# Optimization experiments

Measured on AMD Instinct MI355X. Metric: run time of the kernel, lower is better.

The kernel has to match this reference:

```python
import jax, jax.numpy as jnp
import numpy as np

B, L, NUM_AA, E, H = 128, 2048, 20, 16, 128

def _mlp(x, W1, b1, W2, b2, W3, b3):
    h = jax.nn.relu(x @ W1 + b1)
    h = jax.nn.relu(h @ W2 + b2)
    return h @ W3 + b3

def _mlp_params(key, in_dim):
    k1, k2, k3 = jax.random.split(key, 3)
    W1 = jax.random.normal(k1, (in_dim, H), jnp.float32) / np.sqrt(in_dim)
    W2 = jax.random.normal(k2, (H, H), jnp.float32) / np.sqrt(H)
    W3 = jax.random.normal(k3, (H, 1), jnp.float32) / np.sqrt(H)
    return W1, jnp.zeros((H,), jnp.float32), W2, jnp.zeros((H,), jnp.float32), W3, jnp.zeros((1,), jnp.float32)

def setup_inputs() -> dict:
    key = jax.random.key(0)
    kR, ks, ke, kl, kt, kp = jax.random.split(key, 6)
    inp = {
        'R': jax.random.normal(kR, (B, L, 3), jnp.float32) * 3.8,  # ~CA-CA scale
        'seq': jax.random.randint(ks, (B, L), 0, NUM_AA),
        'emb': jax.random.normal(ke, (NUM_AA, E), jnp.float32),
    }
    for pref, k, d in (('fl', kl, 1 + 2 * E), ('ft', kt, 1 + 3 * E), ('fp', kp, 2 + 4 * E)):
        W1, b1, W2, b2, W3, b3 = _mlp_params(k, d)
        inp.update({f'{pref}_W1': W1, f'{pref}_b1': b1, f'{pref}_W2': W2, f'{pref}_b2': b2, f'{pref}_W3': W3, f'{pref}_b3': b3})
    return inp

def _energy(R, e, fl, ft, fp):
    d = R[:, 1:, :] - R[:, :-1, :]                      # [B,L-1,3] bond vectors
    lengths = jnp.linalg.norm(d, axis=-1)               # [B,L-1]
    x_l = jnp.concatenate([lengths[..., None], e[:, :-1, :], e[:, 1:, :]], axis=-1)
    E_l = _mlp(x_l, *fl)[..., 0].sum(axis=1)
    # bond angles at atom i+1 between (R[i]-R[i+1]) and (R[i+2]-R[i+1])
    u, v = -d[:, :-1, :], d[:, 1:, :]                   # [B,L-2,3]
    cos_t = jnp.sum(u * v, axis=-1) / (jnp.linalg.norm(u, axis=-1) * jnp.linalg.norm(v, axis=-1))
    theta_in = jnp.clip(cos_t, -1.0, 1.0)               # use_cos_theta=True -> cos(arccos(clip))
    x_t = jnp.concatenate([theta_in[..., None], e[:, :-2, :], e[:, 1:-1, :], e[:, 2:, :]], axis=-1)
    E_t = _mlp(x_t, *ft)[..., 0].sum(axis=1)
    # torsions over quadruples
    b1, b2, b3 = d[:, :-2, :], d[:, 1:-1, :], d[:, 2:, :]
    n1 = jnp.cross(b1, b2)
    n2 = jnp.cross(b2, b3)
    b2u = b2 / jnp.linalg.norm(b2, axis=-1, keepdims=True)
    m1 = jnp.cross(n1, b2u)
    phi = jnp.arctan2(jnp.sum(m1 * n2, axis=-1), jnp.sum(n1 * n2, axis=-1))  # [B,L-3]
    sc = jnp.stack([jnp.sin(phi), jnp.cos(phi)], axis=-1)                    # [B,L-3,2]
    x_p = jnp.concatenate([sc, e[:, :-3, :], e[:, 1:-2, :], e[:, 2:-1, :], e[:, 3:, :]], axis=-1)
    E_p = _mlp(x_p, *fp)[..., 0].sum(axis=1)
    return E_l + E_t + E_p

def reference(R, seq, emb,
              fl_W1, fl_b1, fl_W2, fl_b2, fl_W3, fl_b3,
              ft_W1, ft_b1, ft_W2, ft_b2, ft_W3, ft_b3,
              fp_W1, fp_b1, fp_W2, fp_b2, fp_W3, fp_b3):
    e = emb[seq]                                        # [B,L,E]
    return _energy(R, e,
                   (fl_W1, fl_b1, fl_W2, fl_b2, fl_W3, fl_b3),
                   (ft_W1, ft_b1, ft_W2, ft_b2, ft_W3, ft_b3),
                   (fp_W1, fp_b1, fp_W2, fp_b2, fp_W3, fp_b3))
```

## Files before the change

kernel.cpp:

```cpp
#include <hip/hip_runtime.h>


typedef short bf16x8  __attribute__((ext_vector_type(8)));
typedef float f32x4   __attribute__((ext_vector_type(4)));
typedef float f32x16  __attribute__((ext_vector_type(16)));

constexpr int Lc = 2048;

union FragU { uint4 u; bf16x8 v; };

__device__ __forceinline__ unsigned short f2bf(float f) {
    union { float f; unsigned u; } v; v.f = f;
    unsigned u = v.u;
    u = u + 0x7FFFu + ((u >> 16) & 1u);
    return (unsigned short)(u >> 16);
}

__device__ __forceinline__ unsigned pkbf(float a, float b) {
    unsigned ua = __float_as_uint(a) + 0x8000u;
    unsigned ub = __float_as_uint(b) + 0x8000u;
    return __builtin_amdgcn_perm(ub, ua, 0x07060302u);
}

__device__ __forceinline__ void pl32swap(unsigned &a, unsigned &b) {
#if __has_builtin(__builtin_amdgcn_permlane32_swap)
    auto r = __builtin_amdgcn_permlane32_swap(a, b, false, false);
    a = r[0]; b = r[1];
#else
    asm("v_permlane32_swap_b32 %0, %1" : "+v"(a), "+v"(b));
#endif
}

__global__ __launch_bounds__(256)
void prep_kernel(const float* __restrict__ W1_0, const float* __restrict__ b1_0,
                 const float* __restrict__ W1_1, const float* __restrict__ b1_1,
                 const float* __restrict__ W1_2, const float* __restrict__ b1_2,
                 const float* __restrict__ W2_0, const float* __restrict__ W2_1,
                 const float* __restrict__ W2_2,
                 const float* __restrict__ emb, char* __restrict__ ws,
                 float* __restrict__ out)
{
    const int tid = blockIdx.x * 256 + threadIdx.x;
    const int np  = gridDim.x * 256;
    if (blockIdx.x == 0 && threadIdx.x < 128) out[threadIdx.x] = 0.0f;

    unsigned short* d2 = (unsigned short*)ws;
    for (int o = tid; o < 3 * 16384; o += np) {
        int t = o >> 14, r = o & 16383;
        int col = (r >> 3) & 127;
        int k   = ((r >> 10) << 3) | (r & 7);
        const float* W2 = (t == 0) ? W2_0 : (t == 1) ? W2_1 : W2_2;
        d2[o] = f2bf(W2[k * 128 + col]);
    }
    unsigned short* d1 = (unsigned short*)(ws + 98304);
    for (int o = tid; o < 3 * 12288; o += np) {
        int t = o / 12288, r = o - t * 12288;
        int hid = (r >> 3) & 127;
        int k   = ((r >> 10) << 3) | (r & 7);
        const int NE16 = (t == 0) ? 32 : (t == 1) ? 48 : 64;
        const int NG   = (t == 2) ? 2 : 1;
        const float* W1 = (t == 0) ? W1_0 : (t == 1) ? W1_1 : W1_2;
        const float* b1 = (t == 0) ? b1_0 : (t == 1) ? b1_1 : b1_2;
        float v = 0.0f;
        if (k >= 16) {
            int j = k - 16;
            if (j < NE16) v = W1[(NG + j) * 128 + hid];
        } else if (k == 4) v = b1[hid];
        else if (t == 0 && k == 0) v = W1_0[hid];
        else if (t == 1 && k == 1) v = W1_1[hid];
        else if (t == 2 && k == 2) v = W1_2[hid];
        else if (t == 2 && k == 3) v = W1_2[128 + hid];
        d1[o] = f2bf(v);
    }
    unsigned short* eb = (unsigned short*)(ws + 172032);
    for (int i = tid; i < 320; i += np) eb[i] = f2bf(emb[i]);
}

struct SMem {
    float  Rbuf[393];
    uint2  geomh[128];
    int    seqb[132];
    alignas(16) unsigned short ebuf[320];
    float  part[4];
};

template<int TYPE>
__device__ __forceinline__ void type_pass(
    const SMem& sm, const char* __restrict__ ws,
    const float* __restrict__ b2, const float* __restrict__ w3,
    int i0, int wv, int ln31, int hi, f32x4& p4)
{
    constexpr int NEMB  = (TYPE == 0) ? 2 : (TYPE == 1) ? 3 : 4;
    constexpr int STEPS = 1 + NEMB;
    constexpr int ROWSB = Lc - 1 - TYPE;

    const unsigned short* w1t = (const unsigned short*)(ws + 98304 + TYPE * 24576);
    const unsigned short* w2t = (const unsigned short*)(ws + TYPE * 32768);
    const int rloc = wv * 32 + ln31;

    f32x16 acc1[4];
    acc1[0] = (f32x16)(0.f); acc1[1] = (f32x16)(0.f);
    acc1[2] = (f32x16)(0.f); acc1[3] = (f32x16)(0.f);

#pragma unroll
    for (int s = 0; s < STEPS; ++s) {
        FragU bb;
        if (s == 0) {
            if (hi == 0) {
                uint2 g = sm.geomh[rloc];
                bb.u = make_uint4(g.x, g.y, 0x00003F80u, 0u);
            } else {
                bb.u = make_uint4(0u, 0u, 0u, 0u);
            }
        } else {
            bb.u = *(const uint4*)&sm.ebuf[sm.seqb[rloc + (s - 1)] * 16 + hi * 8];
        }
#pragma unroll
        for (int mt = 0; mt < 4; ++mt) {
            FragU A1;
            A1.u = *(const uint4*)&w1t[(((s * 2 + hi) * 128) + mt * 32 + ln31) * 8];
            acc1[mt] = __builtin_amdgcn_mfma_f32_32x32x16_bf16(A1.v, bb.v, acc1[mt], 0, 0, 0);
        }
    }

    FragU a2[8];
#pragma unroll
    for (int mt = 0; mt < 4; ++mt) {
        unsigned P0[4], P1[4];
#pragma unroll
        for (int g = 0; g < 4; ++g) {
            float v0 = fmaxf(acc1[mt][4 * g + 0], 0.f);
            float v1 = fmaxf(acc1[mt][4 * g + 1], 0.f);
            float v2 = fmaxf(acc1[mt][4 * g + 2], 0.f);
            float v3 = fmaxf(acc1[mt][4 * g + 3], 0.f);
            P0[g] = pkbf(v0, v1);
            P1[g] = pkbf(v2, v3);
        }
        unsigned a0 = P0[0], b0 = P0[1]; pl32swap(a0, b0);
        unsigned a1 = P1[0], b1 = P1[1]; pl32swap(a1, b1);
        a2[2 * mt].u     = make_uint4(a0, a1, b0, b1);
        unsigned c0 = P0[2], d0 = P0[3]; pl32swap(c0, d0);
        unsigned c1 = P1[2], d1 = P1[3]; pl32swap(c1, d1);
        a2[2 * mt + 1].u = make_uint4(c0, c1, d0, d1);
    }

    float b2v[4], w3v[4];
#pragma unroll
    for (int nt = 0; nt < 4; ++nt) {
        b2v[nt] = b2[nt * 32 + ln31];
        w3v[nt] = w3[nt * 32 + ln31];
    }

    f32x16 acc2[4];
    acc2[0] = (f32x16)(0.f); acc2[1] = (f32x16)(0.f);
    acc2[2] = (f32x16)(0.f); acc2[3] = (f32x16)(0.f);
#pragma unroll
    for (int s2 = 0; s2 < 8; ++s2) {
#pragma unroll
        for (int nt = 0; nt < 4; ++nt) {
            FragU B2;
            B2.u = *(const uint4*)&w2t[(((s2 * 2 + hi) * 128) + nt * 32 + ln31) * 8];
            acc2[nt] = __builtin_amdgcn_mfma_f32_32x32x16_bf16(a2[s2].v, B2.v, acc2[nt], 0, 0, 0);
        }
    }

    const f32x4 z4 = (f32x4){0.f, 0.f, 0.f, 0.f};
#pragma unroll
    for (int g = 0; g < 4; ++g) {
        const int rbase = i0 + wv * 32 + 8 * g + 4 * hi;
#pragma unroll
        for (int nt = 0; nt < 4; ++nt) {
            f32x4 v;
            v[0] = acc2[nt][4 * g + 0]; v[1] = acc2[nt][4 * g + 1];
            v[2] = acc2[nt][4 * g + 2]; v[3] = acc2[nt][4 * g + 3];
            v = __builtin_elementwise_max(v + b2v[nt], z4);
            if (rbase + 3 < ROWSB) {
                p4 += v * w3v[nt];
            } else {
#pragma unroll
                for (int j = 0; j < 4; ++j)
                    if (rbase + j < ROWSB) p4[j] += v[j] * w3v[nt];
            }
        }
    }
}

__global__ __launch_bounds__(256, 3)
void energy_kernel(const float* __restrict__ R, const int* __restrict__ seq,
                   const char* __restrict__ ws,
                   const float* b2_0, const float* b2_1, const float* b2_2,
                   const float* w3_0, const float* w3_1, const float* w3_2,
                   const float* b3_0, const float* b3_1, const float* b3_2,
                   float* __restrict__ out)
{
    __shared__ SMem sm;
    const int tid = threadIdx.x;
    const int b   = blockIdx.y;
    const int i0  = blockIdx.x * 128;
    const int lane = tid & 63, wv = tid >> 6;
    const int ln31 = lane & 31, hi = lane >> 5;

    for (int t = tid; t < 393; t += 256) {
        int lr = t / 3, comp = t - lr * 3;
        int row = min(i0 + lr, Lc - 1);
        sm.Rbuf[t] = R[((size_t)b * Lc + row) * 3 + comp];
    }
    for (int t = tid; t < 131; t += 256)
        sm.seqb[t] = seq[b * Lc + min(i0 + t, Lc - 1)];
    {
        const uint4* se = (const uint4*)(ws + 172032);
        for (int t = tid; t < 40; t += 256) ((uint4*)sm.ebuf)[t] = se[t];
    }
    __syncthreads();

    if (tid < 128) {
        const float* p0 = &sm.Rbuf[tid * 3];
        float ax = p0[3] - p0[0], ay = p0[4] - p0[1], az = p0[5] - p0[2];
        float bx = p0[6] - p0[3], by = p0[7] - p0[4], bz = p0[8] - p0[5];
        float cx = p0[9] - p0[6], cy = p0[10] - p0[7], cz = p0[11] - p0[8];
        float na2 = ax * ax + ay * ay + az * az;
        float len = sqrtf(na2);
        float nb2 = bx * bx + by * by + bz * bz;
        float duv = -(ax * bx + ay * by + az * bz);
        float cost = fminf(fmaxf(duv / sqrtf(na2 * nb2), -1.0f), 1.0f);
        float n1x = ay * bz - az * by, n1y = az * bx - ax * bz, n1z = ax * by - ay * bx;
        float n2x = by * cz - bz * cy, n2y = bz * cx - bx * cz, n2z = bx * cy - by * cx;
        float binv = 1.0f / sqrtf(nb2);
        float ux = bx * binv, uy = by * binv, uz = bz * binv;
        float m1x = n1y * uz - n1z * uy, m1y = n1z * ux - n1x * uz, m1z = n1x * uy - n1y * ux;
        float yv = m1x * n2x + m1y * n2y + m1z * n2z;
        float xv = n1x * n2x + n1y * n2y + n1z * n2z;
        float inv = 1.0f / sqrtf(xv * xv + yv * yv);
        sm.geomh[tid] = make_uint2(pkbf(len, cost), pkbf(yv * inv, xv * inv));
    }
    __syncthreads();

    f32x4 p4 = (f32x4){0.f, 0.f, 0.f, 0.f};
    type_pass<0>(sm, ws, b2_0, w3_0, i0, wv, ln31, hi, p4);
    type_pass<1>(sm, ws, b2_1, w3_1, i0, wv, ln31, hi, p4);
    type_pass<2>(sm, ws, b2_2, w3_2, i0, wv, ln31, hi, p4);

    float p = p4[0] + p4[1] + p4[2] + p4[3];
#pragma unroll
    for (int off = 32; off > 0; off >>= 1)
        p += __shfl_down(p, off);
    if (lane == 0) sm.part[wv] = p;
    __syncthreads();
    if (tid == 0) {
        float tot = sm.part[0] + sm.part[1] + sm.part[2] + sm.part[3];
        tot += b3_0[0] * (float)min(Lc - 1 - i0, 128);
        tot += b3_1[0] * (float)min(Lc - 2 - i0, 128);
        tot += b3_2[0] * (float)min(Lc - 3 - i0, 128);
        atomicAdd(&out[b], tot);
    }
}

extern "C" void kernel_launch(void* const* d_in, const int* in_sizes, int n_in,
                              void* d_out, int out_size, void* d_ws, size_t ws_size,
                              hipStream_t stream) {
    const float* R   = (const float*)d_in[0];
    const int*   seq = (const int*)d_in[1];
    const float* emb = (const float*)d_in[2];
    float* out = (float*)d_out;
    char*  ws  = (char*)d_ws;

    prep_kernel<<<dim3(96), dim3(256), 0, stream>>>(
        (const float*)d_in[3],  (const float*)d_in[4],
        (const float*)d_in[9],  (const float*)d_in[10],
        (const float*)d_in[15], (const float*)d_in[16],
        (const float*)d_in[5],  (const float*)d_in[11], (const float*)d_in[17],
        emb, ws, out);

    dim3 grid(16, 128), block(256);
    energy_kernel<<<grid, block, 0, stream>>>(
        R, seq, ws,
        (const float*)d_in[6],  (const float*)d_in[12], (const float*)d_in[18],
        (const float*)d_in[7],  (const float*)d_in[13], (const float*)d_in[19],
        (const float*)d_in[8],  (const float*)d_in[14], (const float*)d_in[20],
        out);
}
```

Before: 176.4 us.

## Process four 32-row chunks per wave to reuse weight fragments across rows

Each wave now handles 128 rows (four 32-row chunks) instead of 32, so a block covers 512 rows and the grid shrinks from 16x128 to 4x128 blocks. Layer-1 weight fragments are loaded once per pair of M-tiles and reused across all four row chunks. Layer-2 loops over output tiles, prefetching the next W2 fragment and applying it to all four chunks. This cuts global/L2 weight-fragment traffic per row but raises register pressure (a2 holds 32 fragments), lowers the occupancy bound from 3 to 2 blocks per CU, and launches only 512 blocks, which may underfill the GPU.

```diff
diff --git a/kernel.cpp b/kernel.cpp
--- a/kernel.cpp
+++ b/kernel.cpp
@@ -29,6 +29,25 @@
 #else
     asm("v_permlane32_swap_b32 %0, %1" : "+v"(a), "+v"(b));
 #endif
+}
+
+__device__ __forceinline__ void pack_pair(const f32x16& acc, FragU& f0, FragU& f1) {
+    unsigned P0[4], P1[4];
+#pragma unroll
+    for (int g = 0; g < 4; ++g) {
+        float v0 = fmaxf(acc[4 * g + 0], 0.f);
+        float v1 = fmaxf(acc[4 * g + 1], 0.f);
+        float v2 = fmaxf(acc[4 * g + 2], 0.f);
+        float v3 = fmaxf(acc[4 * g + 3], 0.f);
+        P0[g] = pkbf(v0, v1);
+        P1[g] = pkbf(v2, v3);
+    }
+    unsigned a0 = P0[0], b0 = P0[1]; pl32swap(a0, b0);
+    unsigned a1 = P1[0], b1 = P1[1]; pl32swap(a1, b1);
+    f0.u = make_uint4(a0, a1, b0, b1);
+    unsigned c0 = P0[2], d0 = P0[3]; pl32swap(c0, d0);
+    unsigned c1 = P1[2], d1 = P1[3]; pl32swap(c1, d1);
+    f1.u = make_uint4(c0, c1, d0, d1);
 }
 
 __global__ __launch_bounds__(256)
@@ -77,9 +96,9 @@
 }
 
 struct SMem {
-    float  Rbuf[393];
-    uint2  geomh[128];
-    int    seqb[132];
+    float  Rbuf[1548];
+    uint2  geomh[512];
+    int    seqb[516];
     alignas(16) unsigned short ebuf[320];
     float  part[4];
 };
@@ -96,96 +115,85 @@
 
     const unsigned short* w1t = (const unsigned short*)(ws + 98304 + TYPE * 24576);
     const unsigned short* w2t = (const unsigned short*)(ws + TYPE * 32768);
-    const int rloc = wv * 32 + ln31;
-
-    f32x16 acc1[4];
-    acc1[0] = (f32x16)(0.f); acc1[1] = (f32x16)(0.f);
-    acc1[2] = (f32x16)(0.f); acc1[3] = (f32x16)(0.f);
-
-#pragma unroll
-    for (int s = 0; s < STEPS; ++s) {
-        FragU bb;
-        if (s == 0) {
-            if (hi == 0) {
-                uint2 g = sm.geomh[rloc];
-                bb.u = make_uint4(g.x, g.y, 0x00003F80u, 0u);
-            } else {
-                bb.u = make_uint4(0u, 0u, 0u, 0u);
+
+    FragU a2[4][8];
+
+#pragma unroll
+    for (int mtp = 0; mtp < 2; ++mtp) {
+        FragU A1[STEPS][2];
+#pragma unroll
+        for (int s = 0; s < STEPS; ++s)
+#pragma unroll
+            for (int m = 0; m < 2; ++m)
+                A1[s][m].u = *(const uint4*)&w1t[(((s * 2 + hi) * 128) + (mtp * 2 + m) * 32 + ln31) * 8];
+
+#pragma unroll
+        for (int rc = 0; rc < 4; ++rc) {
+            const int rloc = wv * 128 + rc * 32 + ln31;
+            f32x16 accA = (f32x16)(0.f);
+            f32x16 accB = (f32x16)(0.f);
+#pragma unroll
+            for (int s = 0; s < STEPS; ++s) {
+                FragU bb;
+                if (s == 0) {
+                    if (hi == 0) {
+                        uint2 g = sm.geomh[rloc];
+                        bb.u = make_uint4(g.x, g.y, 0x00003F80u, 0u);
+                    } else {
+                        bb.u = make_uint4(0u, 0u, 0u, 0u);
+                    }
+                } else {
+                    bb.u = *(const uint4*)&sm.ebuf[sm.seqb[rloc + (s - 1)] * 16 + hi * 8];
+                }
+                accA = __builtin_amdgcn_mfma_f32_32x32x16_bf16(A1[s][0].v, bb.v, accA, 0, 0, 0);
+                accB = __builtin_amdgcn_mfma_f32_32x32x16_bf16(A1[s][1].v, bb.v, accB, 0, 0, 0);
             }
-        } else {
-            bb.u = *(const uint4*)&sm.ebuf[sm.seqb[rloc + (s - 1)] * 16 + hi * 8];
+            pack_pair(accA, a2[rc][4 * mtp + 0], a2[rc][4 * mtp + 1]);
+            pack_pair(accB, a2[rc][4 * mtp + 2], a2[rc][4 * mtp + 3]);
         }
-#pragma unroll
-        for (int mt = 0; mt < 4; ++mt) {
-            FragU A1;
-            A1.u = *(const uint4*)&w1t[(((s * 2 + hi) * 128) + mt * 32 + ln31) * 8];
-            acc1[mt] = __builtin_amdgcn_mfma_f32_32x32x16_bf16(A1.v, bb.v, acc1[mt], 0, 0, 0);
+    }
+
+    for (int nt = 0; nt < 4; ++nt) {
+        const float b2v = b2[nt * 32 + ln31];
+        const float w3v = w3[nt * 32 + ln31];
+        f32x16 acc2[4];
+        acc2[0] = (f32x16)(0.f); acc2[1] = (f32x16)(0.f);
+        acc2[2] = (f32x16)(0.f); acc2[3] = (f32x16)(0.f);
+        FragU B2c, B2n;
+        B2c.u = *(const uint4*)&w2t[((hi * 128) + nt * 32 + ln31) * 8];
+#pragma unroll
+        for (int s2 = 0; s2 < 8; ++s2) {
+            if (s2 < 7)
+                B2n.u = *(const uint4*)&w2t[((((s2 + 1) * 2 + hi) * 128) + nt * 32 + ln31) * 8];
+#pragma unroll
+            for (int rc = 0; rc < 4; ++rc)
+                acc2[rc] = __builtin_amdgcn_mfma_f32_32x32x16_bf16(a2[rc][s2].v, B2c.v, acc2[rc], 0, 0, 0);
+            if (s2 < 7) B2c = B2n;
         }
-    }
-
-    FragU a2[8];
-#pragma unroll
-    for (int mt = 0; mt < 4; ++mt) {
-        unsigned P0[4], P1[4];
-#pragma unroll
-        for (int g = 0; g < 4; ++g) {
-            float v0 = fmaxf(acc1[mt][4 * g + 0], 0.f);
-            float v1 = fmaxf(acc1[mt][4 * g + 1], 0.f);
-            float v2 = fmaxf(acc1[mt][4 * g + 2], 0.f);
-            float v3 = fmaxf(acc1[mt][4 * g + 3], 0.f);
-            P0[g] = pkbf(v0, v1);
-            P1[g] = pkbf(v2, v3);
-        }
-        unsigned a0 = P0[0], b0 = P0[1]; pl32swap(a0, b0);
-        unsigned a1 = P1[0], b1 = P1[1]; pl32swap(a1, b1);
-        a2[2 * mt].u     = make_uint4(a0, a1, b0, b1);
-        unsigned c0 = P0[2], d0 = P0[3]; pl32swap(c0, d0);
-        unsigned c1 = P1[2], d1 = P1[3]; pl32swap(c1, d1);
-        a2[2 * mt + 1].u = make_uint4(c0, c1, d0, d1);
-    }
-
-    float b2v[4], w3v[4];
-#pragma unroll
-    for (int nt = 0; nt < 4; ++nt) {
-        b2v[nt] = b2[nt * 32 + ln31];
-        w3v[nt] = w3[nt * 32 + ln31];
-    }
-
-    f32x16 acc2[4];
-    acc2[0] = (f32x16)(0.f); acc2[1] = (f32x16)(0.f);
-    acc2[2] = (f32x16)(0.f); acc2[3] = (f32x16)(0.f);
-#pragma unroll
-    for (int s2 = 0; s2 < 8; ++s2) {
-#pragma unroll
-        for (int nt = 0; nt < 4; ++nt) {
-            FragU B2;
-            B2.u = *(const uint4*)&w2t[(((s2 * 2 + hi) * 128) + nt * 32 + ln31) * 8];
-            acc2[nt] = __builtin_amdgcn_mfma_f32_32x32x16_bf16(a2[s2].v, B2.v, acc2[nt], 0, 0, 0);
-        }
-    }
-
-    const f32x4 z4 = (f32x4){0.f, 0.f, 0.f, 0.f};
-#pragma unroll
-    for (int g = 0; g < 4; ++g) {
-        const int rbase = i0 + wv * 32 + 8 * g + 4 * hi;
-#pragma unroll
-        for (int nt = 0; nt < 4; ++nt) {
-            f32x4 v;
-            v[0] = acc2[nt][4 * g + 0]; v[1] = acc2[nt][4 * g + 1];
-            v[2] = acc2[nt][4 * g + 2]; v[3] = acc2[nt][4 * g + 3];
-            v = __builtin_elementwise_max(v + b2v[nt], z4);
-            if (rbase + 3 < ROWSB) {
-                p4 += v * w3v[nt];
-            } else {
-#pragma unroll
-                for (int j = 0; j < 4; ++j)
-                    if (rbase + j < ROWSB) p4[j] += v[j] * w3v[nt];
+
+        const f32x4 z4 = (f32x4){0.f, 0.f, 0.f, 0.f};
+#pragma unroll
+        for (int rc = 0; rc < 4; ++rc) {
+#pragma unroll
+            for (int g = 0; g < 4; ++g) {
+                const int rbase = i0 + wv * 128 + rc * 32 + 8 * g + 4 * hi;
+                f32x4 v;
+                v[0] = acc2[rc][4 * g + 0]; v[1] = acc2[rc][4 * g + 1];
+                v[2] = acc2[rc][4 * g + 2]; v[3] = acc2[rc][4 * g + 3];
+                v = __builtin_elementwise_max(v + b2v, z4);
+                if (rbase + 3 < ROWSB) {
+                    p4 += v * w3v;
+                } else {
+#pragma unroll
+                    for (int j = 0; j < 4; ++j)
+                        if (rbase + j < ROWSB) p4[j] += v[j] * w3v;
+                }
             }
         }
     }
 }
 
-__global__ __launch_bounds__(256, 3)
+__global__ __launch_bounds__(256, 2)
 void energy_kernel(const float* __restrict__ R, const int* __restrict__ seq,
                    const char* __restrict__ ws,
                    const float* b2_0, const float* b2_1, const float* b2_2,
@@ -196,16 +204,16 @@
     __shared__ SMem sm;
     const int tid = threadIdx.x;
     const int b   = blockIdx.y;
-    const int i0  = blockIdx.x * 128;
+    const int i0  = blockIdx.x * 512;
     const int lane = tid & 63, wv = tid >> 6;
     const int ln31 = lane & 31, hi = lane >> 5;
 
-    for (int t = tid; t < 393; t += 256) {
+    for (int t = tid; t < 1548; t += 256) {
         int lr = t / 3, comp = t - lr * 3;
         int row = min(i0 + lr, Lc - 1);
         sm.Rbuf[t] = R[((size_t)b * Lc + row) * 3 + comp];
     }
-    for (int t = tid; t < 131; t += 256)
+    for (int t = tid; t < 516; t += 256)
         sm.seqb[t] = seq[b * Lc + min(i0 + t, Lc - 1)];
     {
         const uint4* se = (const uint4*)(ws + 172032);
@@ -213,8 +221,8 @@
     }
     __syncthreads();
 
-    if (tid < 128) {
-        const float* p0 = &sm.Rbuf[tid * 3];
+    for (int rr = tid; rr < 512; rr += 256) {
+        const float* p0 = &sm.Rbuf[rr * 3];
         float ax = p0[3] - p0[0], ay = p0[4] - p0[1], az = p0[5] - p0[2];
         float bx = p0[6] - p0[3], by = p0[7] - p0[4], bz = p0[8] - p0[5];
         float cx = p0[9] - p0[6], cy = p0[10] - p0[7], cz = p0[11] - p0[8];
@@ -231,7 +239,7 @@
         float yv = m1x * n2x + m1y * n2y + m1z * n2z;
         float xv = n1x * n2x + n1y * n2y + n1z * n2z;
         float inv = 1.0f / sqrtf(xv * xv + yv * yv);
-        sm.geomh[tid] = make_uint2(pkbf(len, cost), pkbf(yv * inv, xv * inv));
+        sm.geomh[rr] = make_uint2(pkbf(len, cost), pkbf(yv * inv, xv * inv));
     }
     __syncthreads();
 
@@ -248,9 +256,9 @@
     __syncthreads();
     if (tid == 0) {
         float tot = sm.part[0] + sm.part[1] + sm.part[2] + sm.part[3];
-        tot += b3_0[0] * (float)min(Lc - 1 - i0, 128);
-        tot += b3_1[0] * (float)min(Lc - 2 - i0, 128);
-        tot += b3_2[0] * (float)min(Lc - 3 - i0, 128);
+        tot += b3_0[0] * (float)min(Lc - 1 - i0, 512);
+        tot += b3_1[0] * (float)min(Lc - 2 - i0, 512);
+        tot += b3_2[0] * (float)min(Lc - 3 - i0, 512);
         atomicAdd(&out[b], tot);
     }
 }
@@ -271,7 +279,7 @@
         (const float*)d_in[5],  (const float*)d_in[11], (const float*)d_in[17],
         emb, ws, out);
 
-    dim3 grid(16, 128), block(256);
+    dim3 grid(4, 128), block(256);
     energy_kernel<<<grid, block, 0, stream>>>(
         R, seq, ws,
         (const float*)d_in[6],  (const float*)d_in[12], (const float*)d_in[18],
```

After: 171.9 us. 2.5% less time.
